# Optimization experiments

Hardware: AMD Instinct MI355X
Metric: run time of the kernel (lower is better)

## Reference

```python
import jax, jax.numpy as jnp
import numpy as np

EPS = 1e-5


def layer_norm(x, g, b):
    mu = jnp.mean(x, axis=-1, keepdims=True)
    var = jnp.var(x, axis=-1, keepdims=True)
    return (x - mu) * jax.lax.rsqrt(var + EPS) * g + b


def setup_inputs() -> dict:
    key = jax.random.key(0)
    ks = jax.random.split(key, 10)
    B, N, D, H, DFF = 4, 2048, 384, 6, 2048
    s = lambda fan: 1.0 / np.sqrt(fan)
    return {
        "x": jax.random.normal(ks[0], (B, N, D), dtype=jnp.float32),
        "norm_g": jnp.ones((D,), jnp.float32),
        "norm_b": jnp.zeros((D,), jnp.float32),
        "w_qkv": jax.random.uniform(ks[1], (D, 3 * D), jnp.float32, -s(D), s(D)),
        "b_qkv": jax.random.uniform(ks[2], (3 * D,), jnp.float32, -s(D), s(D)),
        "w1": jax.random.uniform(ks[3], (D, DFF), jnp.float32, -s(D), s(D)),
        "b1": jax.random.uniform(ks[4], (DFF,), jnp.float32, -s(D), s(D)),
        "w2": jax.random.uniform(ks[5], (DFF, D), jnp.float32, -s(DFF), s(DFF)),
        "b2": jax.random.uniform(ks[6], (D,), jnp.float32, -s(DFF), s(DFF)),
    }


def reference(x, norm_g, norm_b, w_qkv, b_qkv, w1, b1, w2, b2):
    H = 6
    B, N, D = x.shape
    hd = D // H
    scale = hd ** -0.5

    # --- attention (pre-norm, shared LayerNorm params) ---
    out = layer_norm(x, norm_g, norm_b)
    qkv = out @ w_qkv + b_qkv                     # [B, N, 3D]
    q, k, v = jnp.split(qkv, 3, axis=-1)
    to_heads = lambda t: t.reshape(B, N, H, hd).transpose(0, 2, 1, 3)  # b h n d
    q, k, v = to_heads(q), to_heads(k), to_heads(v)
    scores = jnp.einsum('bhid,bhjd->bhij', q, k) * scale
    attn = jax.nn.softmax(scores, axis=-1)        # dropout is identity in eval
    att = jnp.einsum('bhij,bhjd->bhid', attn, v)  # [B, H, N, hd]
    att = att.transpose(0, 2, 1, 3).reshape(B, N, D)
    x2 = x + att

    # --- MLP (same shared LayerNorm) ---
    y = layer_norm(x2, norm_g, norm_b)
    h = jax.nn.gelu(y @ w1 + b1, approximate=False)  # torch F.gelu exact
    mlp = h @ w2 + b2
    return x2 + mlp
```

## Files before the change

kernel.cpp:

```cpp
#include <hip/hip_runtime.h>
#include <cstdint>
#include <cstddef>

#define DEV static __device__ __forceinline__

typedef __attribute__((ext_vector_type(8))) short short8;
typedef __attribute__((ext_vector_type(4))) float f32x4;
typedef __attribute__((ext_vector_type(4))) unsigned short u16x4;
typedef __attribute__((ext_vector_type(2))) unsigned short u16x2;

constexpr int kB = 4, kN = 2048, kD = 384, kH = 6, kDFF = 2048;
constexpr int kM = kB * kN;
constexpr int kBH = kB * kH;
constexpr float kQPre = 0.18033688011112042f;

DEV float exp2fast(float f) { return __builtin_amdgcn_exp2f(f); }

DEV unsigned short f2b(float f) {
  union { float fp; uint32_t u; } v; v.fp = f;
  return (unsigned short)((v.u + 0x7fffu + ((v.u >> 16) & 1u)) >> 16);
}

DEV void gload16(const unsigned short* g, unsigned short* l) {
  __builtin_amdgcn_global_load_lds(
      (const __attribute__((address_space(1))) unsigned int*)g,
      (__attribute__((address_space(3))) unsigned int*)l, 16, 0, 0);
}

__global__ __launch_bounds__(256) void k_transpose(
    const float* __restrict__ w, unsigned short* __restrict__ wT, int K, int Nn) {
  __shared__ unsigned short t[64][66];
  const int nbk = K >> 6;
  const int bk = blockIdx.x % nbk, bn = blockIdx.x / nbk;
  const int k0 = bk << 6, n0 = bn << 6;
  const int tid = threadIdx.x;
  const int cl = tid & 63, rw = tid >> 6;
#pragma unroll
  for (int it = 0; it < 16; ++it) {
    int kk = it * 4 + rw;
    t[cl][kk] = f2b(w[(size_t)(k0 + kk) * Nn + n0 + cl]);
  }
  __syncthreads();
  const int kq = (tid & 15) << 2;
  const int nr = tid >> 4;
#pragma unroll
  for (int it = 0; it < 4; ++it) {
    int nn = it * 16 + nr;
    u16x4 v;
    v[0] = t[nn][kq]; v[1] = t[nn][kq + 1]; v[2] = t[nn][kq + 2]; v[3] = t[nn][kq + 3];
    *(u16x4*)&wT[(size_t)(n0 + nn) * K + k0 + kq] = v;
  }
}

__global__ __launch_bounds__(256) void k_layernorm(
    const float* __restrict__ x, const float* __restrict__ g,
    const float* __restrict__ bta, unsigned short* __restrict__ y) {
  int row  = blockIdx.x * 4 + (threadIdx.x >> 6);
  int lane = threadIdx.x & 63;
  const float* xr = x + (size_t)row * kD;
  float4 a = *(const float4*)(xr + lane * 4);
  float2 c = *(const float2*)(xr + 256 + lane * 2);
  float s  = a.x + a.y + a.z + a.w + c.x + c.y;
  float ss = a.x*a.x + a.y*a.y + a.z*a.z + a.w*a.w + c.x*c.x + c.y*c.y;
#pragma unroll
  for (int m = 1; m < 64; m <<= 1) {
    s  += __shfl_xor(s,  m, 64);
    ss += __shfl_xor(ss, m, 64);
  }
  float mean = s * (1.0f / kD);
  float var  = ss * (1.0f / kD) - mean * mean;
  float r = rsqrtf(var + 1e-5f);
  float4 g4 = *(const float4*)(g + lane * 4);
  float2 g2 = *(const float2*)(g + 256 + lane * 2);
  float4 b4 = *(const float4*)(bta + lane * 4);
  float2 b2 = *(const float2*)(bta + 256 + lane * 2);
  unsigned short* yr = y + (size_t)row * kD;
  u16x4 o4;
  o4[0] = f2b((a.x - mean) * r * g4.x + b4.x);
  o4[1] = f2b((a.y - mean) * r * g4.y + b4.y);
  o4[2] = f2b((a.z - mean) * r * g4.z + b4.z);
  o4[3] = f2b((a.w - mean) * r * g4.w + b4.w);
  *(u16x4*)(yr + lane * 4) = o4;
  u16x2 o2;
  o2[0] = f2b((c.x - mean) * r * g2.x + b2.x);
  o2[1] = f2b((c.y - mean) * r * g2.y + b2.y);
  *(u16x2*)(yr + 256 + lane * 2) = o2;
}

template <int MODE, int TM>
__global__ __launch_bounds__(256) void k_gemm(
    const unsigned short* __restrict__ A, const unsigned short* __restrict__ Bt,
    const float* __restrict__ bias, int K, int Nn, int nbm,
    unsigned short* __restrict__ oq, unsigned short* __restrict__ okk,
    unsigned short* __restrict__ ov, unsigned short* __restrict__ oh,
    const float* __restrict__ res, float* __restrict__ out) {
  constexpr int MI = TM / 32;
  __shared__ unsigned short lA[2][TM * 32];
  __shared__ unsigned short lB[2][128 * 32];
  const int tid = threadIdx.x, wid = tid >> 6, lane = tid & 63;
  const int bm = blockIdx.x % nbm, bn = blockIdx.x / nbm;
  const int m0 = bm * TM, n0 = bn * 128;
  const int wr = wid >> 1, wc = wid & 1;
  const int wmo = wr * (TM >> 1);
  const int lr16 = lane & 15, lq = lane >> 4;
  const int gsw = ((lr16 >> 1) & 3) << 3;

  f32x4 acc[MI][4];
#pragma unroll
  for (int i = 0; i < MI; i++)
#pragma unroll
    for (int j = 0; j < 4; j++) acc[i][j] = f32x4{0.f, 0.f, 0.f, 0.f};

  const int srow = (lane >> 2);
  const int scc  = (lane & 3) << 3;

  auto stage = [&](int buf, int k0) {
#pragma unroll
    for (int p = 0; p < TM / 64; p++) {
      int row = ((wid + (p << 2)) << 4) + srow;
      int sl  = ((lane & 3) ^ ((row >> 1) & 3)) << 3;
      gload16(A + (size_t)(m0 + row) * K + k0 + sl, &lA[buf][(row << 5) + scc]);
    }
#pragma unroll
    for (int p = 0; p < 2; p++) {
      int row = ((wid + (p << 2)) << 4) + srow;
      int sl  = ((lane & 3) ^ ((row >> 1) & 3)) << 3;
      gload16(Bt + (size_t)(n0 + row) * K + k0 + sl, &lB[buf][(row << 5) + scc]);
    }
  };

  stage(0, 0);

  const int nkt = K >> 5;
  for (int kt = 0; kt < nkt; ++kt) {
    const int cur = kt & 1;
    __syncthreads();
    if (kt + 1 < nkt) stage(cur ^ 1, (kt + 1) << 5);
    short8 af[MI], bf[4];
#pragma unroll
    for (int i = 0; i < MI; i++)
      af[i] = *(const short8*)&lA[cur][(wmo + (i << 4) + lr16) * 32 + ((lq << 3) ^ gsw)];
#pragma unroll
    for (int j = 0; j < 4; j++)
      bf[j] = *(const short8*)&lB[cur][((wc << 6) + (j << 4) + lr16) * 32 + ((lq << 3) ^ gsw)];
#pragma unroll
    for (int i = 0; i < MI; i++)
#pragma unroll
      for (int j = 0; j < 4; j++)
        acc[i][j] = __builtin_amdgcn_mfma_f32_16x16x32_bf16(af[i], bf[j], acc[i][j], 0, 0, 0);
  }

#pragma unroll
  for (int i = 0; i < MI; i++) {
    int mbase = m0 + wmo + (i << 4) + (lq << 2);
#pragma unroll
    for (int j = 0; j < 4; j++) {
      int col = n0 + (wc << 6) + (j << 4) + lr16;
      float bv = bias[col];
#pragma unroll
      for (int rr = 0; rr < 4; ++rr) {
        float cvl = acc[i][j][rr] + bv;
        int m = mbase + rr;
        if (MODE == 0) {
          int bI = m >> 11, nI = m & 2047;
          if (col < 384) {
            int hh = col >> 6, dd = col & 63;
            oq[(((size_t)bI * kH + hh) * kN + nI) * 64 + dd] = f2b(cvl * kQPre);
          } else if (col < 768) {
            int c2 = col - 384; int hh = c2 >> 6, dd = c2 & 63;
            okk[(((size_t)bI * kH + hh) * kN + nI) * 64 + dd] = f2b(cvl);
          } else {
            int c2 = col - 768; int hh = c2 >> 6, dd = c2 & 63;
            ov[(((size_t)bI * kH + hh) * 64 + dd) * kN + nI] = f2b(cvl);
          }
        } else if (MODE == 1) {
          float gl = 0.5f * cvl * (1.0f + erff(cvl * 0.70710678118654752f));
          oh[(size_t)m * kDFF + col] = f2b(gl);
        } else {
          size_t idx = (size_t)m * kD + col;
          out[idx] = res[idx] + cvl;
        }
      }
    }
  }
}

__global__ __launch_bounds__(256) void k_attn(
    const unsigned short* __restrict__ Q, const unsigned short* __restrict__ Kg,
    const unsigned short* __restrict__ Vt, const float* __restrict__ x,
    float* __restrict__ x2) {
  __shared__ unsigned short lK[2][64 * 64];
  __shared__ unsigned short lV[2][64 * 64];
  __shared__ unsigned short lP[4][16 * 64];
  const int tid = threadIdx.x, wid = tid >> 6, lane = tid & 63;
  const int swz = (blockIdx.x & 7) * (gridDim.x >> 3) + (blockIdx.x >> 3);
  const int bh = swz >> 5, qt = swz & 31;
  const int b = bh / kH, h = bh - b * kH;
  const unsigned short* Qp = Q  + (size_t)bh * kN * 64;
  const unsigned short* Kp = Kg + (size_t)bh * kN * 64;
  const unsigned short* Vp = Vt + (size_t)bh * 64 * kN;
  const int lr16 = lane & 15, lq = lane >> 4;
  const int q0w = qt * 64 + wid * 16;
  const int rsw = (lr16 & 7) << 3;

  const int sr  = ((wid << 3) + (lane >> 3));
  const int scc = (lane & 7) << 3;

  short8 qf[2];
#pragma unroll
  for (int ks = 0; ks < 2; ++ks)
    qf[ks] = *(const short8*)(Qp + (size_t)(q0w + lr16) * 64 + ks * 32 + lq * 8);

  const short8 ones = {0x3F80, 0x3F80, 0x3F80, 0x3F80, 0x3F80, 0x3F80, 0x3F80, 0x3F80};
  f32x4 o[4], o_l;
#pragma unroll
  for (int df = 0; df < 4; ++df) o[df] = f32x4{0.f, 0.f, 0.f, 0.f};
  o_l = f32x4{0.f, 0.f, 0.f, 0.f};

  auto stage = [&](int buf, int t) {
#pragma unroll
    for (int p = 0; p < 2; p++) {
      int r = sr + (p << 5);
      int sl = ((lane & 7) ^ (r & 7)) << 3;
      gload16(Kp + (size_t)(t * 64 + r) * 64 + sl, &lK[buf][(r << 6) + scc]);
      gload16(Vp + (size_t)r * kN + t * 64 + sl,   &lV[buf][(r << 6) + scc]);
    }
  };

  stage(0, 0);

  constexpr int kNT = kN / 64;
  for (int t = 0; t < kNT; ++t) {
    const int cur = t & 1;
    __syncthreads();
    if (t + 1 < kNT) stage(cur ^ 1, t + 1);

    f32x4 s4[4];
#pragma unroll
    for (int j = 0; j < 4; j++) {
      s4[j] = f32x4{0.f, 0.f, 0.f, 0.f};
#pragma unroll
      for (int ks = 0; ks < 2; ks++) {
        short8 kf = *(const short8*)&lK[cur][((j << 4) + lr16) * 64 + ((ks * 32 + (lq << 3)) ^ rsw)];
        s4[j] = __builtin_amdgcn_mfma_f32_16x16x32_bf16(kf, qf[ks], s4[j], 0, 0, 0);
      }
    }

#pragma unroll
    for (int j = 0; j < 4; j++) {
      float p0 = exp2fast(s4[j][0]);
      float p1 = exp2fast(s4[j][1]);
      float p2 = exp2fast(s4[j][2]);
      float p3 = exp2fast(s4[j][3]);
      uint32_t w0, w1;
      asm("v_cvt_pk_bf16_f32 %0, %1, %2" : "=v"(w0) : "v"(p0), "v"(p1));
      asm("v_cvt_pk_bf16_f32 %0, %1, %2" : "=v"(w1) : "v"(p2), "v"(p3));
      int kvb = (j << 4) + (lq << 2);
      uint2 wv; wv.x = w0; wv.y = w1;
      *(uint2*)&lP[wid][(lr16 << 6) + (kvb ^ rsw)] = wv;
    }

    short8 pa[2];
#pragma unroll
    for (int ks = 0; ks < 2; ks++)
      pa[ks] = *(const short8*)&lP[wid][(lr16 << 6) + ((ks * 32 + (lq << 3)) ^ rsw)];
#pragma unroll
    for (int ks = 0; ks < 2; ks++)
      o_l = __builtin_amdgcn_mfma_f32_16x16x32_bf16(pa[ks], ones, o_l, 0, 0, 0);
#pragma unroll
    for (int df = 0; df < 4; df++) {
#pragma unroll
      for (int ks = 0; ks < 2; ks++) {
        short8 vf = *(const short8*)&lV[cur][((df << 4) + lr16) * 64 + ((ks * 32 + (lq << 3)) ^ rsw)];
        o[df] = __builtin_amdgcn_mfma_f32_16x16x32_bf16(pa[ks], vf, o[df], 0, 0, 0);
      }
    }
  }

  float inv[4];
#pragma unroll
  for (int rr = 0; rr < 4; rr++) inv[rr] = __builtin_amdgcn_rcpf(o_l[rr]);
#pragma unroll
  for (int df = 0; df < 4; df++)
#pragma unroll
    for (int rr = 0; rr < 4; rr++) {
      int row  = q0w + (lq << 2) + rr;
      int colD = h * 64 + (df << 4) + lr16;
      size_t idx = ((size_t)(b * kN + row)) * kD + colD;
      x2[idx] = x[idx] + o[df][rr] * inv[rr];
    }
}

extern "C" void kernel_launch(void* const* d_in, const int* in_sizes, int n_in,
                              void* d_out, int out_size, void* d_ws, size_t ws_size,
                              hipStream_t stream) {
  const float* x    = (const float*)d_in[0];
  const float* ng   = (const float*)d_in[1];
  const float* nb   = (const float*)d_in[2];
  const float* wqkv = (const float*)d_in[3];
  const float* bqkv = (const float*)d_in[4];
  const float* w1   = (const float*)d_in[5];
  const float* b1   = (const float*)d_in[6];
  const float* w2   = (const float*)d_in[7];
  const float* b2   = (const float*)d_in[8];
  float* out = (float*)d_out;

  char* p = (char*)d_ws;
  auto take = [&](size_t bytes) -> char* {
    char* r = p; p += (bytes + 255) & ~(size_t)255; return r;
  };
  unsigned short* y     = (unsigned short*)take((size_t)kM * kD * 2);
  unsigned short* wqkvT = (unsigned short*)take((size_t)3 * kD * kD * 2);
  unsigned short* w1T   = (unsigned short*)take((size_t)kDFF * kD * 2);
  unsigned short* w2T   = (unsigned short*)take((size_t)kD * kDFF * 2);
  unsigned short* Qw    = (unsigned short*)take((size_t)kM * kD * 2);
  unsigned short* Kw    = (unsigned short*)take((size_t)kM * kD * 2);
  unsigned short* Vtw   = (unsigned short*)take((size_t)kM * kD * 2);
  float*          x2    = (float*)take((size_t)kM * kD * 4);
  unsigned short* hbuf  = (unsigned short*)take((size_t)kM * kDFF * 2);

  k_transpose<<<(kD / 64) * (3 * kD / 64), 256, 0, stream>>>(wqkv, wqkvT, kD, 3 * kD);
  k_transpose<<<(kD / 64) * (kDFF / 64), 256, 0, stream>>>(w1, w1T, kD, kDFF);
  k_transpose<<<(kDFF / 64) * (kD / 64), 256, 0, stream>>>(w2, w2T, kDFF, kD);

  k_layernorm<<<kM / 4, 256, 0, stream>>>(x, ng, nb, y);
  k_gemm<0, 128><<<64 * 9, 256, 0, stream>>>(y, wqkvT, bqkv, kD, 3 * kD, 64,
                                             Qw, Kw, Vtw, nullptr, nullptr, nullptr);
  k_attn<<<kBH * 32, 256, 0, stream>>>(Qw, Kw, Vtw, x, x2);
  k_layernorm<<<kM / 4, 256, 0, stream>>>(x2, ng, nb, y);
  k_gemm<1, 128><<<64 * 16, 256, 0, stream>>>(y, w1T, b1, kD, kDFF, 64,
                                              nullptr, nullptr, nullptr, hbuf, nullptr, nullptr);
  k_gemm<2, 64><<<128 * 3, 256, 0, stream>>>(hbuf, w2T, b2, kDFF, kD, 128,
                                             nullptr, nullptr, nullptr, nullptr, x2, out);
}
```

Measured before the change: 159.8 us.

## Merge weight transposes, shrink GEMM M-tiles, and use fast GELU approximation

Combines the three weight-transpose launches into a single kernel, halves the M tile of the QKV GEMM and the down-projection GEMM (adding a TM=32 staging path) to raise block counts, and replaces the exact erf GELU with an exp2/rcp sigmoid-style approximation. Together these aim to cut launch overhead, fill the GPU better on the smaller GEMMs, and make the epilogue cheaper. The GELU approximation departs from the exact erf form and may shift numerical accuracy. Smaller tiles also mean more weight reloads per output.

```diff
diff --git a/kernel.cpp b/kernel.cpp
--- a/kernel.cpp
+++ b/kernel.cpp
@@ -27,11 +27,22 @@
       (__attribute__((address_space(3))) unsigned int*)l, 16, 0, 0);
 }
 
-__global__ __launch_bounds__(256) void k_transpose(
-    const float* __restrict__ w, unsigned short* __restrict__ wT, int K, int Nn) {
+DEV float gelu_fast(float x) {
+  float t = exp2fast(x * (2.3022081f + 0.1029432f * x * x));
+  return x - x * __builtin_amdgcn_rcpf(t + 1.0f);
+}
+
+__global__ __launch_bounds__(256) void k_transpose3(
+    const float* __restrict__ wqkv, unsigned short* __restrict__ wqkvT,
+    const float* __restrict__ w1,   unsigned short* __restrict__ w1T,
+    const float* __restrict__ w2,   unsigned short* __restrict__ w2T) {
   __shared__ unsigned short t[64][66];
-  const int nbk = K >> 6;
-  const int bk = blockIdx.x % nbk, bn = blockIdx.x / nbk;
+  int idx = blockIdx.x;
+  const float* w; unsigned short* wT; int K, Nn, nbk;
+  if (idx < 108)      { w = wqkv; wT = wqkvT; K = 384;  Nn = 1152; nbk = 6; }
+  else if (idx < 300) { w = w1;   wT = w1T;   K = 384;  Nn = 2048; nbk = 6;  idx -= 108; }
+  else                { w = w2;   wT = w2T;   K = 2048; Nn = 384;  nbk = 32; idx -= 300; }
+  const int bk = idx % nbk, bn = idx / nbk;
   const int k0 = bk << 6, n0 = bn << 6;
   const int tid = threadIdx.x;
   const int cl = tid & 63, rw = tid >> 6;
@@ -94,7 +105,7 @@
     unsigned short* __restrict__ oq, unsigned short* __restrict__ okk,
     unsigned short* __restrict__ ov, unsigned short* __restrict__ oh,
     const float* __restrict__ res, float* __restrict__ out) {
-  constexpr int MI = TM / 32;
+  constexpr int MI = (TM + 31) / 32;
   __shared__ unsigned short lA[2][TM * 32];
   __shared__ unsigned short lB[2][128 * 32];
   const int tid = threadIdx.x, wid = tid >> 6, lane = tid & 63;
@@ -115,11 +126,20 @@
   const int scc  = (lane & 3) << 3;
 
   auto stage = [&](int buf, int k0) {
-#pragma unroll
-    for (int p = 0; p < TM / 64; p++) {
-      int row = ((wid + (p << 2)) << 4) + srow;
-      int sl  = ((lane & 3) ^ ((row >> 1) & 3)) << 3;
-      gload16(A + (size_t)(m0 + row) * K + k0 + sl, &lA[buf][(row << 5) + scc]);
+    if constexpr (TM >= 64) {
+#pragma unroll
+      for (int p = 0; p < TM / 64; p++) {
+        int row = ((wid + (p << 2)) << 4) + srow;
+        int sl  = ((lane & 3) ^ ((row >> 1) & 3)) << 3;
+        gload16(A + (size_t)(m0 + row) * K + k0 + sl, &lA[buf][(row << 5) + scc]);
+      }
+    } else {
+      if (tid < TM * 4) {
+        int row = tid >> 2;
+        int sl  = ((tid & 3) ^ ((row >> 1) & 3)) << 3;
+        gload16(A + (size_t)(m0 + row) * K + k0 + sl,
+                &lA[buf][(row << 5) + ((tid & 3) << 3)]);
+      }
     }
 #pragma unroll
     for (int p = 0; p < 2; p++) {
@@ -174,8 +194,7 @@
             ov[(((size_t)bI * kH + hh) * 64 + dd) * kN + nI] = f2b(cvl);
           }
         } else if (MODE == 1) {
-          float gl = 0.5f * cvl * (1.0f + erff(cvl * 0.70710678118654752f));
-          oh[(size_t)m * kDFF + col] = f2b(gl);
+          oh[(size_t)m * kDFF + col] = f2b(gelu_fast(cvl));
         } else {
           size_t idx = (size_t)m * kD + col;
           out[idx] = res[idx] + cvl;
@@ -319,17 +338,15 @@
   float*          x2    = (float*)take((size_t)kM * kD * 4);
   unsigned short* hbuf  = (unsigned short*)take((size_t)kM * kDFF * 2);
 
-  k_transpose<<<(kD / 64) * (3 * kD / 64), 256, 0, stream>>>(wqkv, wqkvT, kD, 3 * kD);
-  k_transpose<<<(kD / 64) * (kDFF / 64), 256, 0, stream>>>(w1, w1T, kD, kDFF);
-  k_transpose<<<(kDFF / 64) * (kD / 64), 256, 0, stream>>>(w2, w2T, kDFF, kD);
+  k_transpose3<<<492, 256, 0, stream>>>(wqkv, wqkvT, w1, w1T, w2, w2T);
 
   k_layernorm<<<kM / 4, 256, 0, stream>>>(x, ng, nb, y);
-  k_gemm<0, 128><<<64 * 9, 256, 0, stream>>>(y, wqkvT, bqkv, kD, 3 * kD, 64,
+  k_gemm<0, 64><<<128 * 9, 256, 0, stream>>>(y, wqkvT, bqkv, kD, 3 * kD, 128,
                                              Qw, Kw, Vtw, nullptr, nullptr, nullptr);
   k_attn<<<kBH * 32, 256, 0, stream>>>(Qw, Kw, Vtw, x, x2);
   k_layernorm<<<kM / 4, 256, 0, stream>>>(x2, ng, nb, y);
   k_gemm<1, 128><<<64 * 16, 256, 0, stream>>>(y, w1T, b1, kD, kDFF, 64,
                                               nullptr, nullptr, nullptr, hbuf, nullptr, nullptr);
-  k_gemm<2, 64><<<128 * 3, 256, 0, stream>>>(hbuf, w2T, b2, kDFF, kD, 128,
+  k_gemm<2, 32><<<256 * 3, 256, 0, stream>>>(hbuf, w2T, b2, kDFF, kD, 256,
                                              nullptr, nullptr, nullptr, nullptr, x2, out);
 }
```

New measurement: 153.6 us. 1.04x faster.
